# Kernel optimization log

Hardware: AMD Instinct MI355X
Metric: run time of the kernel (lower is better)

## Reference

```python
import jax, jax.numpy as jnp
import numpy as np

STRIDES = (2, 2, 2)  # from init strides
BN_EPS = 1e-3        # keras BatchNormalization default epsilon


def upsample3d(x, s):
    # x: [B, D, H, W, C] -> nearest-neighbor repeat, like keras UpSampling3D
    x = jnp.repeat(x, s[0], axis=1)
    x = jnp.repeat(x, s[1], axis=2)
    return jnp.repeat(x, s[2], axis=3)


def _conv3d_same(xi, wi):
    # xi: [D, H, W, C]; wi: [kd, kh, kw, Cin, Cout] -> SAME, stride 1
    return jax.lax.conv_general_dilated(
        xi[None], wi, window_strides=(1, 1, 1), padding='SAME',
        dimension_numbers=('NDHWC', 'DHWIO', 'NDHWC'))[0]


# per-sample dynamic conv: each batch element uses its own hypernet kernel
per_sample_conv3d = jax.vmap(_conv3d_same, in_axes=(0, 0))


def batchnorm_train(x, gamma, beta):
    # training-mode BN over N,D,H,W axes
    mean = jnp.mean(x, axis=(0, 1, 2, 3), keepdims=True)
    var = jnp.var(x, axis=(0, 1, 2, 3), keepdims=True)
    return gamma * (x - mean) * jax.lax.rsqrt(var + BN_EPS) + beta


def setup_inputs() -> dict:
    key = jax.random.key(0)
    k1, k2, k3, k4 = jax.random.split(key, 4)
    B, D, H, W, Cin, Cmid = 4, 8, 32, 32, 128, 64
    x = jax.random.normal(k1, (B, D, H, W, Cin), dtype=jnp.float32)
    # scale kernels like fan-in init to keep activations sane
    w1 = jax.random.normal(k2, (B, 3, 3, 3, Cin, Cmid), dtype=jnp.float32) * 0.02
    w2 = jax.random.normal(k3, (B, 3, 3, 3, 2 * Cmid, Cmid), dtype=jnp.float32) * 0.02
    skip = jax.random.normal(k4, (B, 2 * D, 2 * H, 2 * W, Cmid), dtype=jnp.float32)
    return {
        'x': x, 'w1': w1, 'w2': w2, 'skip': skip,
        'gamma1': jnp.ones((Cmid,), jnp.float32),
        'beta1': jnp.zeros((Cmid,), jnp.float32),
        'gamma2': jnp.ones((Cmid,), jnp.float32),
        'beta2': jnp.zeros((Cmid,), jnp.float32),
        'training': 1,
    }


def reference(x, w1, w2, skip, gamma1, beta1, gamma2, beta2, training):
    x = upsample3d(x, STRIDES)                       # [B, 2D, 2H, 2W, Cin]
    x = per_sample_conv3d(x, w1)                     # [B, 2D, 2H, 2W, Cmid]
    x = batchnorm_train(x, gamma1, beta1)
    x = jax.nn.relu(x)
    x = jnp.concatenate([x, skip], axis=-1)          # [B, 2D, 2H, 2W, 2*Cmid]
    x = per_sample_conv3d(x, w2)                     # [B, 2D, 2H, 2W, Cmid]
    x = batchnorm_train(x, gamma2, beta2)
    return jax.nn.relu(x)
```

## Files before the change

### kernel.cpp

```cpp
#include <hip/hip_runtime.h>


typedef __attribute__((ext_vector_type(8))) short short8;
typedef __attribute__((ext_vector_type(4))) float f32x4;

__device__ __forceinline__ float bf2f(unsigned short u) {
  union { unsigned int i; float f; } v; v.i = ((unsigned int)u) << 16; return v.f;
}
__device__ __forceinline__ unsigned short f2b(float f) {
  union { float ff; unsigned int u; } v; v.ff = f;
  unsigned int x = v.u;
  return (unsigned short)((x + 0x7FFFu + ((x >> 16) & 1u)) >> 16);
}
__device__ __forceinline__ unsigned int pk2(float a, float b) {
  return (unsigned int)f2b(a) | ((unsigned int)f2b(b) << 16);
}
__device__ __forceinline__ void gload16(const void* g, void* l) {
  __builtin_amdgcn_global_load_lds(
      (const __attribute__((address_space(1))) void*)g,
      (__attribute__((address_space(3))) void*)l, 16, 0, 0);
}

#define ASTR 136
#define WSTR 132

__global__ __launch_bounds__(256) void hg_wt_k(const float* __restrict__ w1,
                                               const float* __restrict__ w2,
                                               unsigned short* __restrict__ wt1,
                                               unsigned short* __restrict__ wt2) {
  __shared__ short T[64 * ASTR];
  int blk = blockIdx.x;
  int sel = blk >= 108;
  const float* w = sel ? w2 : w1;
  unsigned short* wt = sel ? wt2 : wt1;
  int bt = sel ? blk - 108 : blk;
  const float* src = w + (size_t)bt * 8192;
  int tid = threadIdx.x;
  int co = tid & 63;
  int c0 = tid >> 6;
  for (int i = 0; i < 32; ++i) {
    int ci = c0 + (i << 2);
    T[co * ASTR + ci] = (short)f2b(src[(size_t)ci * 64 + co]);
  }
  __syncthreads();
  unsigned short* dst = wt + (size_t)bt * 8192;
  for (int i = 0; i < 4; ++i) {
    int task = tid + (i << 8);
    int row = task >> 4, q = task & 15;
    *(uint4*)(dst + row * 128 + (q << 3)) = *(const uint4*)&T[row * ASTR + (q << 3)];
  }
}

__global__ __launch_bounds__(256) void hg_wc1_k(const float* __restrict__ w1,
                                                unsigned short* __restrict__ wc1) {
  __shared__ short T[64 * ASTR];
  int blk = blockIdx.x;
  int b = blk >> 6, m = blk & 63;
  int dd = m >> 4, hh = (m >> 2) & 3, ww = m & 3;
  const int ks[4] = {0, 1, 0, 2}, kc[4] = {1, 2, 2, 1};
  int tid = threadIdx.x, co = tid & 63, c0 = tid >> 6;
  const float* wb = w1 + (size_t)b * 27 * 8192;
  for (int i = 0; i < 32; ++i) {
    int ci = c0 + (i << 2);
    float s = 0.f;
    for (int a = 0; a < kc[dd]; ++a)
      for (int e = 0; e < kc[hh]; ++e)
        for (int c = 0; c < kc[ww]; ++c) {
          int tap = ((ks[dd] + a) * 3 + ks[hh] + e) * 3 + ks[ww] + c;
          s += wb[(size_t)tap * 8192 + (size_t)ci * 64 + co];
        }
    T[co * ASTR + ci] = (short)f2b(s);
  }
  __syncthreads();
  unsigned short* dst = wc1 + (size_t)blk * 8192;
  for (int i = 0; i < 4; ++i) {
    int task = tid + (i << 8);
    int row = task >> 4, q = task & 15;
    *(uint4*)(dst + row * 128 + (q << 3)) = *(const uint4*)&T[row * ASTR + (q << 3)];
  }
}

__global__ __launch_bounds__(256, 3) void hg_c1p_k(
    const unsigned short* __restrict__ xb, const unsigned short* __restrict__ wc1,
    const unsigned short* __restrict__ zb, unsigned short* __restrict__ outb,
    float* __restrict__ sums) {
  __shared__ short Xl[2 * 100 * 128];
  int tid = threadIdx.x;
  int xcd = blockIdx.x & 7, slot = blockIdx.x >> 3;
  int b = xcd & 3;
  int t = ((xcd >> 2) << 7) + slot;
  int od = t >> 4, hti = (t >> 2) & 3, wti = t & 3;
  int pd = od & 1, md = od >> 1;
  int lane = tid & 63, quad = lane >> 4, l16 = lane & 15;
  int wid = tid >> 6;
  int ph = wid >> 1, pw = wid & 1;

  for (int pl = 0; pl < 2; ++pl) {
    int sd = md + pd - 1 + pl;
    int dok = ((unsigned)sd < 8u);
    for (int i = 0; i < 7; ++i) {
      int task = tid + (i << 8);
      if (task < 1600) {
        int pos = task >> 4, pq = task & 15;
        int q = (pq & 8) | ((pq & 7) ^ (pos & 7));
        int sh = pos / 10, sw = pos - sh * 10;
        int h = (hti << 3) + sh - 1, w = (wti << 3) + sw - 1;
        const unsigned short* src = zb;
        if (dok && (unsigned)h < 32u && (unsigned)w < 32u)
          src = xb + ((((size_t)(b * 8 + sd)) * 32 + h) * 32 + w) * 128 + (q << 3);
        gload16(src, (char*)Xl + ((pl * 1600 + (i << 8) + (tid & 192)) << 4));
      }
    }
  }
  __syncthreads();

  f32x4 acc[4][4];
#pragma unroll
  for (int i = 0; i < 4; ++i)
#pragma unroll
    for (int j = 0; j < 4; ++j) acc[i][j] = (f32x4){0.f, 0.f, 0.f, 0.f};

  const unsigned short* wcb = wc1 + ((size_t)b * 64 + (pd << 5) + (ph << 3) + (pw << 1)) * 8192;

  for (int td = 0; td < 2; ++td) {
    const char* Xp = (const char*)Xl + td * 25600;
    for (int th = 0; th < 2; ++th) {
      int hb = ph + th;
      for (int tw = 0; tw < 2; ++tw) {
        int wb2 = pw + tw;
        const unsigned short* wp = wcb + (size_t)((td << 4) + (th << 2) + tw) * 8192;
#pragma unroll
        for (int ksx = 0; ksx < 4; ++ksx) {
          int cq = (ksx << 2) + quad;
          short8 av[4], bv[4];
#pragma unroll
          for (int mt = 0; mt < 4; ++mt) {
            int pos = ((mt << 1) + (l16 >> 3) + hb) * 10 + (l16 & 7) + wb2;
            int pc = (cq & 8) | ((cq & 7) ^ (pos & 7));
            av[mt] = *(const short8*)(Xp + pos * 256 + (pc << 4));
          }
#pragma unroll
          for (int nt = 0; nt < 4; ++nt)
            bv[nt] = *(const short8*)(wp + ((nt << 4) + l16) * 128 + (cq << 3));
#pragma unroll
          for (int mt = 0; mt < 4; ++mt)
#pragma unroll
            for (int nt = 0; nt < 4; ++nt)
              acc[mt][nt] = __builtin_amdgcn_mfma_f32_16x16x32_bf16(
                  av[mt], bv[nt], acc[mt][nt], 0, 0, 0);
        }
      }
    }
  }

  __syncthreads();
  float* sbf = (float*)Xl;
  int rowb = (b * 16 + od) * 64;
#pragma unroll
  for (int nt = 0; nt < 4; ++nt) {
    int n = (nt << 4) + l16;
    float s = 0.f, q2 = 0.f;
#pragma unroll
    for (int mt = 0; mt < 4; ++mt) {
      int mh = (mt << 1) + (quad >> 1);
      int oh = (((hti << 3) + mh) << 1) + ph;
      size_t rb = (size_t)(rowb + oh) * 64;
#pragma unroll
      for (int r = 0; r < 4; ++r) {
        float v = acc[mt][nt][r];
        int ow = (((wti << 3) + ((quad & 1) << 2) + r) << 1) + pw;
        outb[(rb + ow) * 64 + n] = f2b(v);
        s += v; q2 += v * v;
      }
    }
    s += __shfl_xor(s, 16); s += __shfl_xor(s, 32);
    q2 += __shfl_xor(q2, 16); q2 += __shfl_xor(q2, 32);
    if (quad == 0) { sbf[wid * 128 + n] = s; sbf[wid * 128 + 64 + n] = q2; }
  }
  __syncthreads();
  if (tid < 64) {
    float s = sbf[tid] + sbf[128 + tid] + sbf[256 + tid] + sbf[384 + tid];
    float q2 = sbf[64 + tid] + sbf[192 + tid] + sbf[320 + tid] + sbf[448 + tid];
    atomicAdd(&sums[tid], s);
    atomicAdd(&sums[64 + tid], q2);
  }
}

__global__ __launch_bounds__(256) void hg_convf_k(
    const unsigned short* __restrict__ xb, const unsigned short* __restrict__ y1n,
    const unsigned short* __restrict__ skb, const unsigned short* __restrict__ wt,
    const unsigned short* __restrict__ zb,
    unsigned short* __restrict__ outb, float* __restrict__ outf,
    float* __restrict__ sums, int mode) {
  __shared__ short Al[132 * 128];
  __shared__ short Wl[64 * 128];
  int tid = threadIdx.x;
  int xcd = blockIdx.x & 7, slot = blockIdx.x >> 3;
  int b = xcd & 3;
  int t = ((xcd >> 2) << 8) + slot;
  int m0 = (b << 16) + (t << 7);
  int od  = (t >> 5) & 15;
  int oh0 = (t << 1) & 63;
  int lane = tid & 63, quad = lane >> 4, l16 = lane & 15;
  int wm = (tid >> 6) << 5;

  f32x4 acc[2][4];
  for (int i = 0; i < 2; ++i)
    for (int j = 0; j < 4; ++j) acc[i][j] = (f32x4){0.f, 0.f, 0.f, 0.f};

  const unsigned short* wb = wt + (size_t)b * 27 * 8192;

  for (int kd = 0; kd < 3; ++kd) {
    int ud = od + kd - 1;
    int dok = ((unsigned)ud < 16u);
    for (int kh = 0; kh < 3; ++kh) {
      __syncthreads();
      for (int i = 0; i < 9; ++i) {
        int task = tid + (i << 8);
        if (task < 2112) {
          int pos = task >> 4, pq = task & 15;
          int q = (pq & 8) | ((pq & 7) ^ (pos & 7));
          int g = (pos >= 66) ? 1 : 0;
          int uw = pos - (g ? 66 : 0) - 1;
          int uh = oh0 + g + kh - 1;
          const unsigned short* src = zb;
          if (dok && (unsigned)uh < 64u && (unsigned)uw < 64u) {
            if (mode == 0) {
              src = xb + ((((size_t)(b * 8 + (ud >> 1))) * 32 + (uh >> 1)) * 32 +
                          (uw >> 1)) * 128 + (q << 3);
            } else {
              size_t srow = (((size_t)(b * 16 + ud)) * 64 + uh) * 64 + uw;
              src = (q < 8) ? (y1n + srow * 64 + (q << 3))
                            : (skb + srow * 64 + ((q - 8) << 3));
            }
          }
          gload16(src, (char*)Al + (((i << 8) + (tid & 192)) << 4));
        }
      }
      for (int kw = 0; kw < 3; ++kw) {
        if (kw) __syncthreads();
        int tap = (kd * 3 + kh) * 3 + kw;
        const unsigned short* wsrc = wb + (size_t)tap * 8192;
        {
          int co0 = tid >> 4, pq = tid & 15;
          for (int i = 0; i < 4; ++i) {
            int co = co0 + (i << 4);
            int q = (pq & 8) | ((pq & 7) ^ (co & 7));
            gload16(wsrc + co * 128 + (q << 3),
                    (char*)Wl + (((i << 8) + (tid & 192)) << 4));
          }
        }
        __syncthreads();
        for (int k0 = 0; k0 < 128; k0 += 32) {
          int cq = (k0 >> 3) + quad;
          short8 av[2], bv[4];
          for (int mt = 0; mt < 2; ++mt) {
            int r = wm + (mt << 4) + l16;
            int pos = (r >> 6) * 66 + (r & 63) + kw;
            int pc = (cq & 8) | ((cq & 7) ^ (pos & 7));
            av[mt] = *(const short8*)((const char*)Al + pos * 256 + (pc << 4));
          }
          for (int nt = 0; nt < 4; ++nt) {
            int co = (nt << 4) + l16;
            int pc = (cq & 8) | ((cq & 7) ^ (co & 7));
            bv[nt] = *(const short8*)((const char*)Wl + co * 256 + (pc << 4));
          }
          for (int mt = 0; mt < 2; ++mt)
            for (int nt = 0; nt < 4; ++nt)
              acc[mt][nt] = __builtin_amdgcn_mfma_f32_16x16x32_bf16(
                  av[mt], bv[nt], acc[mt][nt], 0, 0, 0);
        }
      }
    }
  }

  __syncthreads();
  float* sbf = (float*)Al;
  for (int nt = 0; nt < 4; ++nt) {
    int n = (nt << 4) + l16;
    float s = 0.f, q2 = 0.f;
    for (int mt = 0; mt < 2; ++mt) {
      int mbase = m0 + wm + (mt << 4) + (quad << 2);
      for (int r = 0; r < 4; ++r) {
        float v = acc[mt][nt][r];
        size_t o = (size_t)(mbase + r) * 64 + n;
        if (mode == 0) outb[o] = f2b(v);
        else outf[o] = v;
        s += v; q2 += v * v;
      }
    }
    s += __shfl_xor(s, 16); s += __shfl_xor(s, 32);
    q2 += __shfl_xor(q2, 16); q2 += __shfl_xor(q2, 32);
    if (quad == 0) { sbf[(wm >> 5) * 128 + n] = s; sbf[(wm >> 5) * 128 + 64 + n] = q2; }
  }
  __syncthreads();
  if (tid < 64) {
    float s = sbf[tid] + sbf[128 + tid] + sbf[256 + tid] + sbf[384 + tid];
    float q2 = sbf[64 + tid] + sbf[192 + tid] + sbf[320 + tid] + sbf[448 + tid];
    atomicAdd(&sums[tid], s);
    atomicAdd(&sums[64 + tid], q2);
  }
}

__global__ __launch_bounds__(256) void hg_conv_o_k(
    const float* __restrict__ xf, const unsigned short* __restrict__ y1n,
    const float* __restrict__ skip, const float* __restrict__ wf,
    const unsigned short* __restrict__ wt, const float* __restrict__ bn,
    unsigned short* __restrict__ outb, float* __restrict__ outf,
    int mode, int has_wt) {
  __shared__ short Al[132 * ASTR];
  __shared__ short Wl[64 * WSTR];
  __shared__ float sbl[128];
  int tid = threadIdx.x;
  int xcd = blockIdx.x & 7, slot = blockIdx.x >> 3;
  int b = xcd & 3;
  int t = ((xcd >> 2) << 8) + slot;
  int m0 = (b << 16) + (t << 7);
  int od  = (t >> 5) & 15;
  int oh0 = (t << 1) & 63;
  int lane = tid & 63, quad = lane >> 4, l16 = lane & 15;
  int wm = (tid >> 6) << 5;

  if (mode == 1 && tid < 128) sbl[tid] = bn[tid];

  f32x4 acc[2][4];
  for (int i = 0; i < 2; ++i)
    for (int j = 0; j < 4; ++j) acc[i][j] = (f32x4){0.f, 0.f, 0.f, 0.f};

  const float* wbf = wf + (size_t)b * 27 * 8192;
  const unsigned short* wbt = wt + (size_t)b * 27 * 8192;

  for (int kd = 0; kd < 3; ++kd) {
    int ud = od + kd - 1;
    int dok = (ud >= 0 && ud < 16);
    for (int kh = 0; kh < 3; ++kh) {
      __syncthreads();
      for (int i = 0; i < 9; ++i) {
        int task = tid + (i << 8);
        if (task < 2112) {
          int chunk = task & 15;
          int pos = task >> 4;
          int g = (pos >= 66) ? 1 : 0;
          int uwi = pos - (g ? 66 : 0);
          int uh = oh0 + g + kh - 1;
          int uw = uwi - 1;
          uint4 val = make_uint4(0u, 0u, 0u, 0u);
          if (dok && (unsigned)uh < 64u && (unsigned)uw < 64u) {
            if (mode == 0) {
              size_t src = ((((size_t)(b * 8 + (ud >> 1))) * 32 + (uh >> 1)) * 32 +
                            (uw >> 1)) * 128 + (chunk << 3);
              float4 f0 = *(const float4*)(xf + src);
              float4 f1 = *(const float4*)(xf + src + 4);
              val.x = pk2(f0.x, f0.y); val.y = pk2(f0.z, f0.w);
              val.z = pk2(f1.x, f1.y); val.w = pk2(f1.z, f1.w);
            } else {
              size_t srow = (((size_t)(b * 16 + ud)) * 64 + uh) * 64 + uw;
              if (chunk < 8) {
                uint4 raw = *(const uint4*)(y1n + srow * 64 + (chunk << 3));
                unsigned int u[4] = {raw.x, raw.y, raw.z, raw.w};
                unsigned int o[4];
                int c0 = chunk << 3;
                for (int q = 0; q < 4; ++q) {
                  int c = c0 + q * 2;
                  float f0 = sbl[c] * bf2f((unsigned short)(u[q] & 0xFFFFu)) + sbl[64 + c];
                  float f1 = sbl[c + 1] * bf2f((unsigned short)(u[q] >> 16)) + sbl[64 + c + 1];
                  o[q] = pk2(f0 > 0.f ? f0 : 0.f, f1 > 0.f ? f1 : 0.f);
                }
                val = make_uint4(o[0], o[1], o[2], o[3]);
              } else {
                const float* sp = skip + srow * 64 + ((chunk - 8) << 3);
                float4 f0 = *(const float4*)(sp);
                float4 f1 = *(const float4*)(sp + 4);
                val.x = pk2(f0.x, f0.y); val.y = pk2(f0.z, f0.w);
                val.z = pk2(f1.x, f1.y); val.w = pk2(f1.z, f1.w);
              }
            }
          }
          *(uint4*)&Al[pos * ASTR + (chunk << 3)] = val;
        }
      }
      for (int kw = 0; kw < 3; ++kw) {
        if (kw) __syncthreads();
        int tap = (kd * 3 + kh) * 3 + kw;
        if (has_wt) {
          const unsigned short* wsrc = wbt + (size_t)tap * 8192;
          for (int i = 0; i < 4; ++i) {
            int task = tid + (i << 8);
            int co = task >> 4, q = task & 15;
            *(uint4*)&Wl[co * WSTR + (q << 3)] = *(const uint4*)(wsrc + co * 128 + (q << 3));
          }
        } else {
          const float* wp = wbf + (size_t)tap * 8192 + (tid & 63);
          int wco = tid & 63;
          int ci0 = (tid >> 6) << 5;
          for (int c = 0; c < 32; c += 2) {
            float f0 = wp[(size_t)(ci0 + c) * 64];
            float f1 = wp[(size_t)(ci0 + c + 1) * 64];
            *(unsigned int*)&Wl[wco * WSTR + ci0 + c] = pk2(f0, f1);
          }
        }
        __syncthreads();
        for (int k0 = 0; k0 < 128; k0 += 32) {
          int kk = k0 + (quad << 3);
          union { uint4 u; short8 s; } cv;
          short8 av[2];
          for (int mt = 0; mt < 2; ++mt) {
            int r = wm + (mt << 4) + l16;
            int g = r >> 6, ow = r & 63;
            cv.u = *(const uint4*)&Al[(g * 66 + ow + kw) * ASTR + kk];
            av[mt] = cv.s;
          }
          short8 bv[4];
          for (int nt = 0; nt < 4; ++nt) {
            int base = ((nt << 4) + l16) * WSTR + kk;
            uint2 lo = *(const uint2*)&Wl[base];
            uint2 hi = *(const uint2*)&Wl[base + 4];
            cv.u = make_uint4(lo.x, lo.y, hi.x, hi.y);
            bv[nt] = cv.s;
          }
          for (int mt = 0; mt < 2; ++mt)
            for (int nt = 0; nt < 4; ++nt)
              acc[mt][nt] = __builtin_amdgcn_mfma_f32_16x16x32_bf16(
                  av[mt], bv[nt], acc[mt][nt], 0, 0, 0);
        }
      }
    }
  }

  for (int mt = 0; mt < 2; ++mt) {
    int mbase = m0 + wm + (mt << 4) + (quad << 2);
    for (int nt = 0; nt < 4; ++nt) {
      int n = (nt << 4) + l16;
      for (int r = 0; r < 4; ++r) {
        float v = acc[mt][nt][r];
        size_t o = (size_t)(mbase + r) * 64 + n;
        if (mode == 0) outb[o] = f2b(v);
        else outf[o] = v;
      }
    }
  }
}

__global__ void hg_zero_k(float* __restrict__ p, int n) {
  for (int i = threadIdx.x; i < n; i += 256) p[i] = 0.f;
}

__global__ __launch_bounds__(256) void hg_stats_k(const unsigned short* __restrict__ yb,
                                                  const float* __restrict__ yf, int isf,
                                                  float* __restrict__ sums) {
  int t = threadIdx.x;
  int c = t & 63;
  int r0 = blockIdx.x * 4 + (t >> 6);
  float sum = 0.f, ss = 0.f;
  for (int r = r0; r < 262144; r += 4096) {
    size_t idx = (size_t)r * 64 + c;
    float v = isf ? yf[idx] : bf2f(yb[idx]);
    sum += v; ss += v * v;
  }
  atomicAdd(&sums[c], sum);
  atomicAdd(&sums[64 + c], ss);
}

__global__ void hg_fin_k(float* __restrict__ sb, const float* __restrict__ gm,
                         const float* __restrict__ bt) {
  int c = threadIdx.x;
  float invN = 1.f / 262144.f;
  float mean = sb[c] * invN;
  float var  = sb[64 + c] * invN - mean * mean;
  float sc = gm[c] * rsqrtf(var + 1e-3f);
  sb[c] = sc;
  sb[64 + c] = bt[c] - mean * sc;
}

__global__ __launch_bounds__(256) void hg_cvt_k(const float* __restrict__ s,
                                                unsigned short* __restrict__ d) {
  size_t i = ((size_t)blockIdx.x * 256 + threadIdx.x) << 3;
  float4 a = *(const float4*)(s + i);
  float4 c = *(const float4*)(s + i + 4);
  uint4 o;
  o.x = pk2(a.x, a.y); o.y = pk2(a.z, a.w);
  o.z = pk2(c.x, c.y); o.w = pk2(c.z, c.w);
  *(uint4*)(d + i) = o;
}

__global__ __launch_bounds__(256) void hg_bnb_k(unsigned short* __restrict__ y,
                                                const float* __restrict__ sb) {
  size_t i = ((size_t)blockIdx.x * 256 + threadIdx.x) << 3;
  int c0 = (int)(i & 63);
  uint4 v = *(uint4*)(y + i);
  unsigned int u[4] = {v.x, v.y, v.z, v.w};
  for (int q = 0; q < 4; ++q) {
    int c = c0 + q * 2;
    float f0 = sb[c] * bf2f((unsigned short)(u[q] & 0xFFFFu)) + sb[64 + c];
    float f1 = sb[c + 1] * bf2f((unsigned short)(u[q] >> 16)) + sb[64 + c + 1];
    u[q] = pk2(f0 > 0.f ? f0 : 0.f, f1 > 0.f ? f1 : 0.f);
  }
  *(uint4*)(y + i) = make_uint4(u[0], u[1], u[2], u[3]);
}

__global__ __launch_bounds__(256) void hg_bnrelu_f_k(float* __restrict__ y,
                                                     const float* __restrict__ sb) {
  size_t i = (size_t)blockIdx.x * 256 + threadIdx.x;
  int c4 = ((int)i & 15) << 2;
  float4 v = *(float4*)(y + i * 4);
  float f;
  f = sb[c4]     * v.x + sb[64 + c4];     v.x = f > 0.f ? f : 0.f;
  f = sb[c4 + 1] * v.y + sb[64 + c4 + 1]; v.y = f > 0.f ? f : 0.f;
  f = sb[c4 + 2] * v.z + sb[64 + c4 + 2]; v.z = f > 0.f ? f : 0.f;
  f = sb[c4 + 3] * v.w + sb[64 + c4 + 3]; v.w = f > 0.f ? f : 0.f;
  *(float4*)(y + i * 4) = v;
}

extern "C" void kernel_launch(void* const* d_in, const int* in_sizes, int n_in,
                              void* d_out, int out_size, void* d_ws, size_t ws_size,
                              hipStream_t stream) {
  (void)out_size;
  int ix = 0, iw1 = 1, iw2 = 2, isk = 3, ig1 = 4, ib1 = 5, ig2 = 6, ib2 = 7;
  if (n_in >= 9 && in_sizes[0] == 4194304 && in_sizes[1] == 884736 &&
      in_sizes[3] == 16777216 && in_sizes[4] == 64) {
  } else if (n_in >= 9 && in_sizes[0] == 64 && in_sizes[4] == 16777216 &&
             in_sizes[6] == 884736 && in_sizes[8] == 4194304) {
    ib1 = 0; ib2 = 1; ig1 = 2; ig2 = 3; isk = 4; iw1 = 6; iw2 = 7; ix = 8;
  } else {
    return;
  }
  if (ws_size < (32ull << 20) + 2048ull) return;

  const float* x    = (const float*)d_in[ix];
  const float* w1   = (const float*)d_in[iw1];
  const float* w2   = (const float*)d_in[iw2];
  const float* skip = (const float*)d_in[isk];
  const float* g1   = (const float*)d_in[ig1];
  const float* b1   = (const float*)d_in[ib1];
  const float* g2   = (const float*)d_in[ig2];
  const float* b2   = (const float*)d_in[ib2];
  float* out = (float*)d_out;

  const size_t OFF_SUMS = 32ull << 20;
  const size_t OFF_ZB   = OFF_SUMS + 2048;
  const size_t OFF_WT1  = OFF_ZB + 256;
  const size_t OFF_WT2  = OFF_WT1 + 1769472;
  const size_t OFF_XB   = OFF_WT2 + 1769472;
  const size_t OFF_SKB  = OFF_XB + 8388608;
  const size_t OFF_WC1  = OFF_SKB + 33554432;
  const size_t NEED     = OFF_WC1 + 4194304;

  unsigned short* y1 = (unsigned short*)d_ws;
  float* sums  = (float*)((char*)d_ws + OFF_SUMS);
  float* sums1 = sums;
  float* sums2 = sums + 128;

  if (ws_size >= NEED) {
    unsigned short* zb  = (unsigned short*)((char*)d_ws + OFF_ZB);
    unsigned short* wt1 = (unsigned short*)((char*)d_ws + OFF_WT1);
    unsigned short* wt2 = (unsigned short*)((char*)d_ws + OFF_WT2);
    unsigned short* xb  = (unsigned short*)((char*)d_ws + OFF_XB);
    unsigned short* skb = (unsigned short*)((char*)d_ws + OFF_SKB);
    unsigned short* wc1 = (unsigned short*)((char*)d_ws + OFF_WC1);

    hg_zero_k<<<1, 256, 0, stream>>>(sums, 576);
    hg_wt_k<<<216, 256, 0, stream>>>(w1, w2, wt1, wt2);
    hg_wc1_k<<<256, 256, 0, stream>>>(w1, wc1);
    hg_cvt_k<<<2048, 256, 0, stream>>>(x, xb);
    hg_cvt_k<<<8192, 256, 0, stream>>>(skip, skb);
    hg_c1p_k<<<1024, 256, 0, stream>>>(xb, wc1, zb, y1, sums1);
    hg_fin_k<<<1, 64, 0, stream>>>(sums1, g1, b1);
    hg_bnb_k<<<8192, 256, 0, stream>>>(y1, sums1);
    hg_convf_k<<<2048, 256, 0, stream>>>(xb, y1, skb, wt2, zb, y1, out, sums2, 1);
    hg_fin_k<<<1, 64, 0, stream>>>(sums2, g2, b2);
    hg_bnrelu_f_k<<<16384, 256, 0, stream>>>(out, sums2);
  } else {
    unsigned short* wt1 = (unsigned short*)((char*)d_ws + (32ull << 20) + 2048ull);
    unsigned short* wt2 = wt1 + 884736ull;
    const size_t WS_NEED = (32ull << 20) + 2048ull + 2ull * 884736ull * 2ull;
    int has_wt = (ws_size >= WS_NEED) ? 1 : 0;

    hg_zero_k<<<1, 256, 0, stream>>>(sums, 512);
    if (has_wt) hg_wt_k<<<216, 256, 0, stream>>>(w1, w2, wt1, wt2);
    hg_conv_o_k<<<2048, 256, 0, stream>>>(x, y1, skip, w1, wt1, sums1, y1, out, 0, has_wt);
    hg_stats_k<<<1024, 256, 0, stream>>>(y1, out, 0, sums1);
    hg_fin_k<<<1, 64, 0, stream>>>(sums1, g1, b1);
    hg_conv_o_k<<<2048, 256, 0, stream>>>(x, y1, skip, w2, wt2, sums1, y1, out, 1, has_wt);
    hg_stats_k<<<1024, 256, 0, stream>>>(y1, out, 1, sums2);
    hg_fin_k<<<1, 64, 0, stream>>>(sums2, g2, b2);
    hg_bnrelu_f_k<<<16384, 256, 0, stream>>>(out, sums2);
  }
}
```

Baseline: 462.6 us.

## Fuse prep kernels, fold BN finalize into apply kernels, spread stat atomics

Merges the zeroing, w2 transpose, folded-w1 build and both bf16 conversions into one multi-role prep kernel, and drops the unused wt1 transpose on the fast path. BN finalize is computed per block inside the BN-apply kernels, which removes the separate single-block finalize launches. The conv kernels now accumulate their statistics into eight per-XCD slots to reduce atomic contention, and the second conv is specialized to drop the mode branches. The aim is fewer launches and serialization gaps. The cost is that every BN-apply block recomputes the finalize, and the workspace layout changes.

```diff
diff --git a/kernel.cpp b/kernel.cpp
--- a/kernel.cpp
+++ b/kernel.cpp
@@ -23,6 +23,341 @@
 
 #define ASTR 136
 #define WSTR 132
+
+__global__ __launch_bounds__(256) void hg_prep_k(
+    const float* __restrict__ x, const float* __restrict__ skip,
+    const float* __restrict__ w1, const float* __restrict__ w2,
+    unsigned short* __restrict__ xb, unsigned short* __restrict__ skb,
+    unsigned short* __restrict__ wt2, unsigned short* __restrict__ wc1,
+    float* __restrict__ sums) {
+  __shared__ short T[64 * ASTR];
+  int blk = blockIdx.x;
+  int tid = threadIdx.x;
+  if (blk < 10240) {
+    const float* s; unsigned short* d; size_t i;
+    if (blk < 8192) { s = skip; d = skb; i = ((size_t)blk * 256 + tid) << 3; }
+    else            { s = x;    d = xb;  i = ((size_t)(blk - 8192) * 256 + tid) << 3; }
+    float4 a = *(const float4*)(s + i);
+    float4 c = *(const float4*)(s + i + 4);
+    uint4 o;
+    o.x = pk2(a.x, a.y); o.y = pk2(a.z, a.w);
+    o.z = pk2(c.x, c.y); o.w = pk2(c.z, c.w);
+    *(uint4*)(d + i) = o;
+  } else if (blk < 10348) {
+    int bt = blk - 10240;
+    const float* src = w2 + (size_t)bt * 8192;
+    int co = tid & 63, c0 = tid >> 6;
+    for (int i = 0; i < 32; ++i) {
+      int ci = c0 + (i << 2);
+      T[co * ASTR + ci] = (short)f2b(src[(size_t)ci * 64 + co]);
+    }
+    __syncthreads();
+    unsigned short* dst = wt2 + (size_t)bt * 8192;
+    for (int i = 0; i < 4; ++i) {
+      int task = tid + (i << 8);
+      int row = task >> 4, q = task & 15;
+      *(uint4*)(dst + row * 128 + (q << 3)) = *(const uint4*)&T[row * ASTR + (q << 3)];
+    }
+  } else if (blk < 10604) {
+    int m9 = blk - 10348;
+    int b = m9 >> 6, m = m9 & 63;
+    int dd = m >> 4, hh = (m >> 2) & 3, ww = m & 3;
+    const int ks[4] = {0, 1, 0, 2}, kc[4] = {1, 2, 2, 1};
+    int co = tid & 63, c0 = tid >> 6;
+    const float* wb = w1 + (size_t)b * 27 * 8192;
+    for (int i = 0; i < 32; ++i) {
+      int ci = c0 + (i << 2);
+      float s = 0.f;
+      for (int a = 0; a < kc[dd]; ++a)
+        for (int e = 0; e < kc[hh]; ++e)
+          for (int c = 0; c < kc[ww]; ++c) {
+            int tap = ((ks[dd] + a) * 3 + ks[hh] + e) * 3 + ks[ww] + c;
+            s += wb[(size_t)tap * 8192 + (size_t)ci * 64 + co];
+          }
+      T[co * ASTR + ci] = (short)f2b(s);
+    }
+    __syncthreads();
+    unsigned short* dst = wc1 + (size_t)m9 * 8192;
+    for (int i = 0; i < 4; ++i) {
+      int task = tid + (i << 8);
+      int row = task >> 4, q = task & 15;
+      *(uint4*)(dst + row * 128 + (q << 3)) = *(const uint4*)&T[row * ASTR + (q << 3)];
+    }
+  } else {
+    for (int i = tid; i < 2112; i += 256) sums[i] = 0.f;
+  }
+}
+
+__global__ __launch_bounds__(256, 3) void hg_c1p_k(
+    const unsigned short* __restrict__ xb, const unsigned short* __restrict__ wc1,
+    const unsigned short* __restrict__ zb, unsigned short* __restrict__ outb,
+    float* __restrict__ sums) {
+  __shared__ short Xl[2 * 100 * 128];
+  int tid = threadIdx.x;
+  int xcd = blockIdx.x & 7, slot = blockIdx.x >> 3;
+  int b = xcd & 3;
+  int t = ((xcd >> 2) << 7) + slot;
+  int od = t >> 4, hti = (t >> 2) & 3, wti = t & 3;
+  int pd = od & 1, md = od >> 1;
+  int lane = tid & 63, quad = lane >> 4, l16 = lane & 15;
+  int wid = tid >> 6;
+  int ph = wid >> 1, pw = wid & 1;
+
+  for (int pl = 0; pl < 2; ++pl) {
+    int sd = md + pd - 1 + pl;
+    int dok = ((unsigned)sd < 8u);
+    for (int i = 0; i < 7; ++i) {
+      int task = tid + (i << 8);
+      if (task < 1600) {
+        int pos = task >> 4, pq = task & 15;
+        int q = (pq & 8) | ((pq & 7) ^ (pos & 7));
+        int sh = pos / 10, sw = pos - sh * 10;
+        int h = (hti << 3) + sh - 1, w = (wti << 3) + sw - 1;
+        const unsigned short* src = zb;
+        if (dok && (unsigned)h < 32u && (unsigned)w < 32u)
+          src = xb + ((((size_t)(b * 8 + sd)) * 32 + h) * 32 + w) * 128 + (q << 3);
+        gload16(src, (char*)Xl + ((pl * 1600 + (i << 8) + (tid & 192)) << 4));
+      }
+    }
+  }
+  __syncthreads();
+
+  f32x4 acc[4][4];
+#pragma unroll
+  for (int i = 0; i < 4; ++i)
+#pragma unroll
+    for (int j = 0; j < 4; ++j) acc[i][j] = (f32x4){0.f, 0.f, 0.f, 0.f};
+
+  const unsigned short* wcb = wc1 + ((size_t)b * 64 + (pd << 5) + (ph << 3) + (pw << 1)) * 8192;
+
+  for (int td = 0; td < 2; ++td) {
+    const char* Xp = (const char*)Xl + td * 25600;
+    for (int th = 0; th < 2; ++th) {
+      int hb = ph + th;
+      for (int tw = 0; tw < 2; ++tw) {
+        int wb2 = pw + tw;
+        const unsigned short* wp = wcb + (size_t)((td << 4) + (th << 2) + tw) * 8192;
+#pragma unroll
+        for (int ksx = 0; ksx < 4; ++ksx) {
+          int cq = (ksx << 2) + quad;
+          short8 av[4], bv[4];
+#pragma unroll
+          for (int mt = 0; mt < 4; ++mt) {
+            int pos = ((mt << 1) + (l16 >> 3) + hb) * 10 + (l16 & 7) + wb2;
+            int pc = (cq & 8) | ((cq & 7) ^ (pos & 7));
+            av[mt] = *(const short8*)(Xp + pos * 256 + (pc << 4));
+          }
+#pragma unroll
+          for (int nt = 0; nt < 4; ++nt)
+            bv[nt] = *(const short8*)(wp + ((nt << 4) + l16) * 128 + (cq << 3));
+#pragma unroll
+          for (int mt = 0; mt < 4; ++mt)
+#pragma unroll
+            for (int nt = 0; nt < 4; ++nt)
+              acc[mt][nt] = __builtin_amdgcn_mfma_f32_16x16x32_bf16(
+                  av[mt], bv[nt], acc[mt][nt], 0, 0, 0);
+        }
+      }
+    }
+  }
+
+  __syncthreads();
+  float* sbf = (float*)Xl;
+  int rowb = (b * 16 + od) * 64;
+#pragma unroll
+  for (int nt = 0; nt < 4; ++nt) {
+    int n = (nt << 4) + l16;
+    float s = 0.f, q2 = 0.f;
+#pragma unroll
+    for (int mt = 0; mt < 4; ++mt) {
+      int mh = (mt << 1) + (quad >> 1);
+      int oh = (((hti << 3) + mh) << 1) + ph;
+      size_t rb = (size_t)(rowb + oh) * 64;
+#pragma unroll
+      for (int r = 0; r < 4; ++r) {
+        float v = acc[mt][nt][r];
+        int ow = (((wti << 3) + ((quad & 1) << 2) + r) << 1) + pw;
+        outb[(rb + ow) * 64 + n] = f2b(v);
+        s += v; q2 += v * v;
+      }
+    }
+    s += __shfl_xor(s, 16); s += __shfl_xor(s, 32);
+    q2 += __shfl_xor(q2, 16); q2 += __shfl_xor(q2, 32);
+    if (quad == 0) { sbf[wid * 128 + n] = s; sbf[wid * 128 + 64 + n] = q2; }
+  }
+  __syncthreads();
+  if (tid < 64) {
+    float s = sbf[tid] + sbf[128 + tid] + sbf[256 + tid] + sbf[384 + tid];
+    float q2 = sbf[64 + tid] + sbf[192 + tid] + sbf[320 + tid] + sbf[448 + tid];
+    int sl = (blockIdx.x & 7) << 7;
+    atomicAdd(&sums[sl + tid], s);
+    atomicAdd(&sums[sl + 64 + tid], q2);
+  }
+}
+
+__global__ __launch_bounds__(256) void hg_convf_k(
+    const unsigned short* __restrict__ y1n, const unsigned short* __restrict__ skb,
+    const unsigned short* __restrict__ wt, const unsigned short* __restrict__ zb,
+    float* __restrict__ outf, float* __restrict__ sums) {
+  __shared__ short Al[132 * 128];
+  __shared__ short Wl[64 * 128];
+  int tid = threadIdx.x;
+  int xcd = blockIdx.x & 7, slot = blockIdx.x >> 3;
+  int b = xcd & 3;
+  int t = ((xcd >> 2) << 8) + slot;
+  int m0 = (b << 16) + (t << 7);
+  int od  = (t >> 5) & 15;
+  int oh0 = (t << 1) & 63;
+  int lane = tid & 63, quad = lane >> 4, l16 = lane & 15;
+  int wm = (tid >> 6) << 5;
+
+  f32x4 acc[2][4];
+  for (int i = 0; i < 2; ++i)
+    for (int j = 0; j < 4; ++j) acc[i][j] = (f32x4){0.f, 0.f, 0.f, 0.f};
+
+  const unsigned short* wb = wt + (size_t)b * 27 * 8192;
+
+  for (int kd = 0; kd < 3; ++kd) {
+    int ud = od + kd - 1;
+    int dok = ((unsigned)ud < 16u);
+    for (int kh = 0; kh < 3; ++kh) {
+      __syncthreads();
+      for (int i = 0; i < 9; ++i) {
+        int task = tid + (i << 8);
+        if (task < 2112) {
+          int pos = task >> 4, pq = task & 15;
+          int q = (pq & 8) | ((pq & 7) ^ (pos & 7));
+          int g = (pos >= 66) ? 1 : 0;
+          int uw = pos - (g ? 66 : 0) - 1;
+          int uh = oh0 + g + kh - 1;
+          const unsigned short* src = zb;
+          if (dok && (unsigned)uh < 64u && (unsigned)uw < 64u) {
+            size_t srow = (((size_t)(b * 16 + ud)) * 64 + uh) * 64 + uw;
+            src = (q < 8) ? (y1n + srow * 64 + (q << 3))
+                          : (skb + srow * 64 + ((q - 8) << 3));
+          }
+          gload16(src, (char*)Al + (((i << 8) + (tid & 192)) << 4));
+        }
+      }
+      for (int kw = 0; kw < 3; ++kw) {
+        if (kw) __syncthreads();
+        int tap = (kd * 3 + kh) * 3 + kw;
+        const unsigned short* wsrc = wb + (size_t)tap * 8192;
+        {
+          int co0 = tid >> 4, pq = tid & 15;
+          for (int i = 0; i < 4; ++i) {
+            int co = co0 + (i << 4);
+            int q = (pq & 8) | ((pq & 7) ^ (co & 7));
+            gload16(wsrc + co * 128 + (q << 3),
+                    (char*)Wl + (((i << 8) + (tid & 192)) << 4));
+          }
+        }
+        __syncthreads();
+        for (int k0 = 0; k0 < 128; k0 += 32) {
+          int cq = (k0 >> 3) + quad;
+          short8 av[2], bv[4];
+          for (int mt = 0; mt < 2; ++mt) {
+            int r = wm + (mt << 4) + l16;
+            int pos = (r >> 6) * 66 + (r & 63) + kw;
+            int pc = (cq & 8) | ((cq & 7) ^ (pos & 7));
+            av[mt] = *(const short8*)((const char*)Al + pos * 256 + (pc << 4));
+          }
+          for (int nt = 0; nt < 4; ++nt) {
+            int co = (nt << 4) + l16;
+            int pc = (cq & 8) | ((cq & 7) ^ (co & 7));
+            bv[nt] = *(const short8*)((const char*)Wl + co * 256 + (pc << 4));
+          }
+          for (int mt = 0; mt < 2; ++mt)
+            for (int nt = 0; nt < 4; ++nt)
+              acc[mt][nt] = __builtin_amdgcn_mfma_f32_16x16x32_bf16(
+                  av[mt], bv[nt], acc[mt][nt], 0, 0, 0);
+        }
+      }
+    }
+  }
+
+  __syncthreads();
+  float* sbf = (float*)Al;
+  for (int nt = 0; nt < 4; ++nt) {
+    int n = (nt << 4) + l16;
+    float s = 0.f, q2 = 0.f;
+    for (int mt = 0; mt < 2; ++mt) {
+      int mbase = m0 + wm + (mt << 4) + (quad << 2);
+      for (int r = 0; r < 4; ++r) {
+        float v = acc[mt][nt][r];
+        outf[(size_t)(mbase + r) * 64 + n] = v;
+        s += v; q2 += v * v;
+      }
+    }
+    s += __shfl_xor(s, 16); s += __shfl_xor(s, 32);
+    q2 += __shfl_xor(q2, 16); q2 += __shfl_xor(q2, 32);
+    if (quad == 0) { sbf[(wm >> 5) * 128 + n] = s; sbf[(wm >> 5) * 128 + 64 + n] = q2; }
+  }
+  __syncthreads();
+  if (tid < 64) {
+    float s = sbf[tid] + sbf[128 + tid] + sbf[256 + tid] + sbf[384 + tid];
+    float q2 = sbf[64 + tid] + sbf[192 + tid] + sbf[320 + tid] + sbf[448 + tid];
+    int sl = (blockIdx.x & 7) << 7;
+    atomicAdd(&sums[sl + tid], s);
+    atomicAdd(&sums[sl + 64 + tid], q2);
+  }
+}
+
+__global__ __launch_bounds__(256) void hg_bnbf_k(unsigned short* __restrict__ y,
+                                                 const float* __restrict__ sb,
+                                                 const float* __restrict__ gm,
+                                                 const float* __restrict__ bt) {
+  __shared__ float sc[64], sh[64];
+  int tid = threadIdx.x;
+  if (tid < 64) {
+    float s = 0.f, q2 = 0.f;
+    for (int k = 0; k < 8; ++k) { s += sb[(k << 7) + tid]; q2 += sb[(k << 7) + 64 + tid]; }
+    float invN = 1.f / 262144.f;
+    float mean = s * invN;
+    float var  = q2 * invN - mean * mean;
+    float scl = gm[tid] * rsqrtf(var + 1e-3f);
+    sc[tid] = scl; sh[tid] = bt[tid] - mean * scl;
+  }
+  __syncthreads();
+  size_t i = ((size_t)blockIdx.x * 256 + tid) << 3;
+  int c0 = (int)(i & 63);
+  uint4 v = *(uint4*)(y + i);
+  unsigned int u[4] = {v.x, v.y, v.z, v.w};
+  for (int q = 0; q < 4; ++q) {
+    int c = c0 + q * 2;
+    float f0 = sc[c] * bf2f((unsigned short)(u[q] & 0xFFFFu)) + sh[c];
+    float f1 = sc[c + 1] * bf2f((unsigned short)(u[q] >> 16)) + sh[c + 1];
+    u[q] = pk2(f0 > 0.f ? f0 : 0.f, f1 > 0.f ? f1 : 0.f);
+  }
+  *(uint4*)(y + i) = make_uint4(u[0], u[1], u[2], u[3]);
+}
+
+__global__ __launch_bounds__(256) void hg_bnrf_k(float* __restrict__ y,
+                                                 const float* __restrict__ sb,
+                                                 const float* __restrict__ gm,
+                                                 const float* __restrict__ bt) {
+  __shared__ float sc[64], sh[64];
+  int tid = threadIdx.x;
+  if (tid < 64) {
+    float s = 0.f, q2 = 0.f;
+    for (int k = 0; k < 8; ++k) { s += sb[(k << 7) + tid]; q2 += sb[(k << 7) + 64 + tid]; }
+    float invN = 1.f / 262144.f;
+    float mean = s * invN;
+    float var  = q2 * invN - mean * mean;
+    float scl = gm[tid] * rsqrtf(var + 1e-3f);
+    sc[tid] = scl; sh[tid] = bt[tid] - mean * scl;
+  }
+  __syncthreads();
+  size_t i = (size_t)blockIdx.x * 256 + tid;
+  int c4 = ((int)i & 15) << 2;
+  float4 v = *(float4*)(y + i * 4);
+  float f;
+  f = sc[c4]     * v.x + sh[c4];     v.x = f > 0.f ? f : 0.f;
+  f = sc[c4 + 1] * v.y + sh[c4 + 1]; v.y = f > 0.f ? f : 0.f;
+  f = sc[c4 + 2] * v.z + sh[c4 + 2]; v.z = f > 0.f ? f : 0.f;
+  f = sc[c4 + 3] * v.w + sh[c4 + 3]; v.w = f > 0.f ? f : 0.f;
+  *(float4*)(y + i * 4) = v;
+}
 
 __global__ __launch_bounds__(256) void hg_wt_k(const float* __restrict__ w1,
                                                const float* __restrict__ w2,
@@ -48,257 +383,6 @@
     int task = tid + (i << 8);
     int row = task >> 4, q = task & 15;
     *(uint4*)(dst + row * 128 + (q << 3)) = *(const uint4*)&T[row * ASTR + (q << 3)];
-  }
-}
-
-__global__ __launch_bounds__(256) void hg_wc1_k(const float* __restrict__ w1,
-                                                unsigned short* __restrict__ wc1) {
-  __shared__ short T[64 * ASTR];
-  int blk = blockIdx.x;
-  int b = blk >> 6, m = blk & 63;
-  int dd = m >> 4, hh = (m >> 2) & 3, ww = m & 3;
-  const int ks[4] = {0, 1, 0, 2}, kc[4] = {1, 2, 2, 1};
-  int tid = threadIdx.x, co = tid & 63, c0 = tid >> 6;
-  const float* wb = w1 + (size_t)b * 27 * 8192;
-  for (int i = 0; i < 32; ++i) {
-    int ci = c0 + (i << 2);
-    float s = 0.f;
-    for (int a = 0; a < kc[dd]; ++a)
-      for (int e = 0; e < kc[hh]; ++e)
-        for (int c = 0; c < kc[ww]; ++c) {
-          int tap = ((ks[dd] + a) * 3 + ks[hh] + e) * 3 + ks[ww] + c;
-          s += wb[(size_t)tap * 8192 + (size_t)ci * 64 + co];
-        }
-    T[co * ASTR + ci] = (short)f2b(s);
-  }
-  __syncthreads();
-  unsigned short* dst = wc1 + (size_t)blk * 8192;
-  for (int i = 0; i < 4; ++i) {
-    int task = tid + (i << 8);
-    int row = task >> 4, q = task & 15;
-    *(uint4*)(dst + row * 128 + (q << 3)) = *(const uint4*)&T[row * ASTR + (q << 3)];
-  }
-}
-
-__global__ __launch_bounds__(256, 3) void hg_c1p_k(
-    const unsigned short* __restrict__ xb, const unsigned short* __restrict__ wc1,
-    const unsigned short* __restrict__ zb, unsigned short* __restrict__ outb,
-    float* __restrict__ sums) {
-  __shared__ short Xl[2 * 100 * 128];
-  int tid = threadIdx.x;
-  int xcd = blockIdx.x & 7, slot = blockIdx.x >> 3;
-  int b = xcd & 3;
-  int t = ((xcd >> 2) << 7) + slot;
-  int od = t >> 4, hti = (t >> 2) & 3, wti = t & 3;
-  int pd = od & 1, md = od >> 1;
-  int lane = tid & 63, quad = lane >> 4, l16 = lane & 15;
-  int wid = tid >> 6;
-  int ph = wid >> 1, pw = wid & 1;
-
-  for (int pl = 0; pl < 2; ++pl) {
-    int sd = md + pd - 1 + pl;
-    int dok = ((unsigned)sd < 8u);
-    for (int i = 0; i < 7; ++i) {
-      int task = tid + (i << 8);
-      if (task < 1600) {
-        int pos = task >> 4, pq = task & 15;
-        int q = (pq & 8) | ((pq & 7) ^ (pos & 7));
-        int sh = pos / 10, sw = pos - sh * 10;
-        int h = (hti << 3) + sh - 1, w = (wti << 3) + sw - 1;
-        const unsigned short* src = zb;
-        if (dok && (unsigned)h < 32u && (unsigned)w < 32u)
-          src = xb + ((((size_t)(b * 8 + sd)) * 32 + h) * 32 + w) * 128 + (q << 3);
-        gload16(src, (char*)Xl + ((pl * 1600 + (i << 8) + (tid & 192)) << 4));
-      }
-    }
-  }
-  __syncthreads();
-
-  f32x4 acc[4][4];
-#pragma unroll
-  for (int i = 0; i < 4; ++i)
-#pragma unroll
-    for (int j = 0; j < 4; ++j) acc[i][j] = (f32x4){0.f, 0.f, 0.f, 0.f};
-
-  const unsigned short* wcb = wc1 + ((size_t)b * 64 + (pd << 5) + (ph << 3) + (pw << 1)) * 8192;
-
-  for (int td = 0; td < 2; ++td) {
-    const char* Xp = (const char*)Xl + td * 25600;
-    for (int th = 0; th < 2; ++th) {
-      int hb = ph + th;
-      for (int tw = 0; tw < 2; ++tw) {
-        int wb2 = pw + tw;
-        const unsigned short* wp = wcb + (size_t)((td << 4) + (th << 2) + tw) * 8192;
-#pragma unroll
-        for (int ksx = 0; ksx < 4; ++ksx) {
-          int cq = (ksx << 2) + quad;
-          short8 av[4], bv[4];
-#pragma unroll
-          for (int mt = 0; mt < 4; ++mt) {
-            int pos = ((mt << 1) + (l16 >> 3) + hb) * 10 + (l16 & 7) + wb2;
-            int pc = (cq & 8) | ((cq & 7) ^ (pos & 7));
-            av[mt] = *(const short8*)(Xp + pos * 256 + (pc << 4));
-          }
-#pragma unroll
-          for (int nt = 0; nt < 4; ++nt)
-            bv[nt] = *(const short8*)(wp + ((nt << 4) + l16) * 128 + (cq << 3));
-#pragma unroll
-          for (int mt = 0; mt < 4; ++mt)
-#pragma unroll
-            for (int nt = 0; nt < 4; ++nt)
-              acc[mt][nt] = __builtin_amdgcn_mfma_f32_16x16x32_bf16(
-                  av[mt], bv[nt], acc[mt][nt], 0, 0, 0);
-        }
-      }
-    }
-  }
-
-  __syncthreads();
-  float* sbf = (float*)Xl;
-  int rowb = (b * 16 + od) * 64;
-#pragma unroll
-  for (int nt = 0; nt < 4; ++nt) {
-    int n = (nt << 4) + l16;
-    float s = 0.f, q2 = 0.f;
-#pragma unroll
-    for (int mt = 0; mt < 4; ++mt) {
-      int mh = (mt << 1) + (quad >> 1);
-      int oh = (((hti << 3) + mh) << 1) + ph;
-      size_t rb = (size_t)(rowb + oh) * 64;
-#pragma unroll
-      for (int r = 0; r < 4; ++r) {
-        float v = acc[mt][nt][r];
-        int ow = (((wti << 3) + ((quad & 1) << 2) + r) << 1) + pw;
-        outb[(rb + ow) * 64 + n] = f2b(v);
-        s += v; q2 += v * v;
-      }
-    }
-    s += __shfl_xor(s, 16); s += __shfl_xor(s, 32);
-    q2 += __shfl_xor(q2, 16); q2 += __shfl_xor(q2, 32);
-    if (quad == 0) { sbf[wid * 128 + n] = s; sbf[wid * 128 + 64 + n] = q2; }
-  }
-  __syncthreads();
-  if (tid < 64) {
-    float s = sbf[tid] + sbf[128 + tid] + sbf[256 + tid] + sbf[384 + tid];
-    float q2 = sbf[64 + tid] + sbf[192 + tid] + sbf[320 + tid] + sbf[448 + tid];
-    atomicAdd(&sums[tid], s);
-    atomicAdd(&sums[64 + tid], q2);
-  }
-}
-
-__global__ __launch_bounds__(256) void hg_convf_k(
-    const unsigned short* __restrict__ xb, const unsigned short* __restrict__ y1n,
-    const unsigned short* __restrict__ skb, const unsigned short* __restrict__ wt,
-    const unsigned short* __restrict__ zb,
-    unsigned short* __restrict__ outb, float* __restrict__ outf,
-    float* __restrict__ sums, int mode) {
-  __shared__ short Al[132 * 128];
-  __shared__ short Wl[64 * 128];
-  int tid = threadIdx.x;
-  int xcd = blockIdx.x & 7, slot = blockIdx.x >> 3;
-  int b = xcd & 3;
-  int t = ((xcd >> 2) << 8) + slot;
-  int m0 = (b << 16) + (t << 7);
-  int od  = (t >> 5) & 15;
-  int oh0 = (t << 1) & 63;
-  int lane = tid & 63, quad = lane >> 4, l16 = lane & 15;
-  int wm = (tid >> 6) << 5;
-
-  f32x4 acc[2][4];
-  for (int i = 0; i < 2; ++i)
-    for (int j = 0; j < 4; ++j) acc[i][j] = (f32x4){0.f, 0.f, 0.f, 0.f};
-
-  const unsigned short* wb = wt + (size_t)b * 27 * 8192;
-
-  for (int kd = 0; kd < 3; ++kd) {
-    int ud = od + kd - 1;
-    int dok = ((unsigned)ud < 16u);
-    for (int kh = 0; kh < 3; ++kh) {
-      __syncthreads();
-      for (int i = 0; i < 9; ++i) {
-        int task = tid + (i << 8);
-        if (task < 2112) {
-          int pos = task >> 4, pq = task & 15;
-          int q = (pq & 8) | ((pq & 7) ^ (pos & 7));
-          int g = (pos >= 66) ? 1 : 0;
-          int uw = pos - (g ? 66 : 0) - 1;
-          int uh = oh0 + g + kh - 1;
-          const unsigned short* src = zb;
-          if (dok && (unsigned)uh < 64u && (unsigned)uw < 64u) {
-            if (mode == 0) {
-              src = xb + ((((size_t)(b * 8 + (ud >> 1))) * 32 + (uh >> 1)) * 32 +
-                          (uw >> 1)) * 128 + (q << 3);
-            } else {
-              size_t srow = (((size_t)(b * 16 + ud)) * 64 + uh) * 64 + uw;
-              src = (q < 8) ? (y1n + srow * 64 + (q << 3))
-                            : (skb + srow * 64 + ((q - 8) << 3));
-            }
-          }
-          gload16(src, (char*)Al + (((i << 8) + (tid & 192)) << 4));
-        }
-      }
-      for (int kw = 0; kw < 3; ++kw) {
-        if (kw) __syncthreads();
-        int tap = (kd * 3 + kh) * 3 + kw;
-        const unsigned short* wsrc = wb + (size_t)tap * 8192;
-        {
-          int co0 = tid >> 4, pq = tid & 15;
-          for (int i = 0; i < 4; ++i) {
-            int co = co0 + (i << 4);
-            int q = (pq & 8) | ((pq & 7) ^ (co & 7));
-            gload16(wsrc + co * 128 + (q << 3),
-                    (char*)Wl + (((i << 8) + (tid & 192)) << 4));
-          }
-        }
-        __syncthreads();
-        for (int k0 = 0; k0 < 128; k0 += 32) {
-          int cq = (k0 >> 3) + quad;
-          short8 av[2], bv[4];
-          for (int mt = 0; mt < 2; ++mt) {
-            int r = wm + (mt << 4) + l16;
-            int pos = (r >> 6) * 66 + (r & 63) + kw;
-            int pc = (cq & 8) | ((cq & 7) ^ (pos & 7));
-            av[mt] = *(const short8*)((const char*)Al + pos * 256 + (pc << 4));
-          }
-          for (int nt = 0; nt < 4; ++nt) {
-            int co = (nt << 4) + l16;
-            int pc = (cq & 8) | ((cq & 7) ^ (co & 7));
-            bv[nt] = *(const short8*)((const char*)Wl + co * 256 + (pc << 4));
-          }
-          for (int mt = 0; mt < 2; ++mt)
-            for (int nt = 0; nt < 4; ++nt)
-              acc[mt][nt] = __builtin_amdgcn_mfma_f32_16x16x32_bf16(
-                  av[mt], bv[nt], acc[mt][nt], 0, 0, 0);
-        }
-      }
-    }
-  }
-
-  __syncthreads();
-  float* sbf = (float*)Al;
-  for (int nt = 0; nt < 4; ++nt) {
-    int n = (nt << 4) + l16;
-    float s = 0.f, q2 = 0.f;
-    for (int mt = 0; mt < 2; ++mt) {
-      int mbase = m0 + wm + (mt << 4) + (quad << 2);
-      for (int r = 0; r < 4; ++r) {
-        float v = acc[mt][nt][r];
-        size_t o = (size_t)(mbase + r) * 64 + n;
-        if (mode == 0) outb[o] = f2b(v);
-        else outf[o] = v;
-        s += v; q2 += v * v;
-      }
-    }
-    s += __shfl_xor(s, 16); s += __shfl_xor(s, 32);
-    q2 += __shfl_xor(q2, 16); q2 += __shfl_xor(q2, 32);
-    if (quad == 0) { sbf[(wm >> 5) * 128 + n] = s; sbf[(wm >> 5) * 128 + 64 + n] = q2; }
-  }
-  __syncthreads();
-  if (tid < 64) {
-    float s = sbf[tid] + sbf[128 + tid] + sbf[256 + tid] + sbf[384 + tid];
-    float q2 = sbf[64 + tid] + sbf[192 + tid] + sbf[320 + tid] + sbf[448 + tid];
-    atomicAdd(&sums[tid], s);
-    atomicAdd(&sums[64 + tid], q2);
   }
 }
 
@@ -472,17 +556,6 @@
   sb[64 + c] = bt[c] - mean * sc;
 }
 
-__global__ __launch_bounds__(256) void hg_cvt_k(const float* __restrict__ s,
-                                                unsigned short* __restrict__ d) {
-  size_t i = ((size_t)blockIdx.x * 256 + threadIdx.x) << 3;
-  float4 a = *(const float4*)(s + i);
-  float4 c = *(const float4*)(s + i + 4);
-  uint4 o;
-  o.x = pk2(a.x, a.y); o.y = pk2(a.z, a.w);
-  o.z = pk2(c.x, c.y); o.w = pk2(c.z, c.w);
-  *(uint4*)(d + i) = o;
-}
-
 __global__ __launch_bounds__(256) void hg_bnb_k(unsigned short* __restrict__ y,
                                                 const float* __restrict__ sb) {
   size_t i = ((size_t)blockIdx.x * 256 + threadIdx.x) << 3;
@@ -537,39 +610,34 @@
   float* out = (float*)d_out;
 
   const size_t OFF_SUMS = 32ull << 20;
-  const size_t OFF_ZB   = OFF_SUMS + 2048;
-  const size_t OFF_WT1  = OFF_ZB + 256;
-  const size_t OFF_WT2  = OFF_WT1 + 1769472;
-  const size_t OFF_XB   = OFF_WT2 + 1769472;
+  const size_t OFF_ZB   = OFF_SUMS + 8192;
+  const size_t OFF_WT2  = OFF_ZB + 256;
+  const size_t OFF_XB   = OFF_WT2 + 2ull * 1769472;
   const size_t OFF_SKB  = OFF_XB + 8388608;
   const size_t OFF_WC1  = OFF_SKB + 33554432;
   const size_t NEED     = OFF_WC1 + 4194304;
 
   unsigned short* y1 = (unsigned short*)d_ws;
-  float* sums  = (float*)((char*)d_ws + OFF_SUMS);
-  float* sums1 = sums;
-  float* sums2 = sums + 128;
 
   if (ws_size >= NEED) {
+    float* sums  = (float*)((char*)d_ws + OFF_SUMS);
+    float* sums1 = sums;
+    float* sums2 = sums + 1024;
     unsigned short* zb  = (unsigned short*)((char*)d_ws + OFF_ZB);
-    unsigned short* wt1 = (unsigned short*)((char*)d_ws + OFF_WT1);
     unsigned short* wt2 = (unsigned short*)((char*)d_ws + OFF_WT2);
     unsigned short* xb  = (unsigned short*)((char*)d_ws + OFF_XB);
     unsigned short* skb = (unsigned short*)((char*)d_ws + OFF_SKB);
     unsigned short* wc1 = (unsigned short*)((char*)d_ws + OFF_WC1);
 
-    hg_zero_k<<<1, 256, 0, stream>>>(sums, 576);
-    hg_wt_k<<<216, 256, 0, stream>>>(w1, w2, wt1, wt2);
-    hg_wc1_k<<<256, 256, 0, stream>>>(w1, wc1);
-    hg_cvt_k<<<2048, 256, 0, stream>>>(x, xb);
-    hg_cvt_k<<<8192, 256, 0, stream>>>(skip, skb);
+    hg_prep_k<<<10605, 256, 0, stream>>>(x, skip, w1, w2, xb, skb, wt2, wc1, sums);
     hg_c1p_k<<<1024, 256, 0, stream>>>(xb, wc1, zb, y1, sums1);
-    hg_fin_k<<<1, 64, 0, stream>>>(sums1, g1, b1);
-    hg_bnb_k<<<8192, 256, 0, stream>>>(y1, sums1);
-    hg_convf_k<<<2048, 256, 0, stream>>>(xb, y1, skb, wt2, zb, y1, out, sums2, 1);
-    hg_fin_k<<<1, 64, 0, stream>>>(sums2, g2, b2);
-    hg_bnrelu_f_k<<<16384, 256, 0, stream>>>(out, sums2);
+    hg_bnbf_k<<<8192, 256, 0, stream>>>(y1, sums1, g1, b1);
+    hg_convf_k<<<2048, 256, 0, stream>>>(y1, skb, wt2, zb, out, sums2);
+    hg_bnrf_k<<<16384, 256, 0, stream>>>(out, sums2, g2, b2);
   } else {
+    float* sums  = (float*)((char*)d_ws + (32ull << 20));
+    float* sums1 = sums;
+    float* sums2 = sums + 128;
     unsigned short* wt1 = (unsigned short*)((char*)d_ws + (32ull << 20) + 2048ull);
     unsigned short* wt2 = wt1 + 884736ull;
     const size_t WS_NEED = (32ull << 20) + 2048ull + 2ull * 884736ull * 2ull;
```

After: 423.5 us. -8.5%, faster.
